# Kernel optimization log

Hardware: AMD Instinct MI355X
Metric: run time of the kernel (lower is better)

## Reference

```python
import jax, jax.numpy as jnp
import numpy as np

NEG_INF = -9e15  # matches torch's -9000000000000000.0 mask value
LEAKY_SLOPE = 0.2  # alpha init arg


def setup_inputs() -> dict:
    key = jax.random.key(0)
    k1, k2, k3, k4, k5, k6 = jax.random.split(key, 6)
    B, N, D = 512, 200, 256
    hidden = jax.random.normal(k1, (B, N, D), dtype=jnp.float32)
    adj = jax.random.randint(k2, (B, N, N), 0, 5, dtype=jnp.int32)
    a0 = jax.random.normal(k3, (D,), dtype=jnp.float32)
    a1 = jax.random.normal(k4, (D,), dtype=jnp.float32)
    a2 = jax.random.normal(k5, (D,), dtype=jnp.float32)
    a3 = jax.random.normal(k6, (D,), dtype=jnp.float32)
    return {"hidden": hidden, "adj": adj, "a0": a0, "a1": a1, "a2": a2, "a3": a3}


def reference(hidden, adj, a0, a1, a2, a3):
    # e_k[b,i,j] = leakyrelu( sum_d h[b,i,d] * h[b,j,d] * a_k[d] )
    # Algebraically identical to the torch (h_i * h_j) @ a_k without
    # materializing the [B, N, N, D] pairwise product tensor.
    def edge_score(a):
        s = jnp.einsum('bid,bjd->bij', hidden * a, hidden)
        return jax.nn.leaky_relu(s, LEAKY_SLOPE)

    e0, e1, e2, e3 = edge_score(a0), edge_score(a1), edge_score(a2), edge_score(a3)
    alpha = jnp.where(adj == 1, e0, NEG_INF)
    alpha = jnp.where(adj == 2, e1, alpha)
    alpha = jnp.where(adj == 3, e2, alpha)
    alpha = jnp.where(adj == 4, e3, alpha)
    alpha = jax.nn.softmax(alpha, axis=-1)  # [B, N, N]
    return jnp.matmul(alpha, hidden)  # [B, N, D]
```

## Files before the change

kernel.cpp:

```cpp
#include <hip/hip_runtime.h>

#define NB 512
#define NN 200
#define ND 256
#define TI 40
#define DC 16
#define NTILE 5
#define NEG_INF -9.0e15f
#define SLOPE 0.2f

#define HJ_STRIDE 204
#define WI_STRIDE 44
#define P1_HJ (DC * HJ_STRIDE)
#define P1_W  (4 * DC * WI_STRIDE)
#define POOLF 8000

__global__ __launch_bounds__(512, 4)
void gat_fused_w3_kernel(const float* __restrict__ h,
                         const int*   __restrict__ adj,
                         const float* __restrict__ a0,
                         const float* __restrict__ a1,
                         const float* __restrict__ a2,
                         const float* __restrict__ a3,
                         float* __restrict__ out)
{
    __shared__ __align__(16) float pool[POOLF];
    float (*sHjT)[HJ_STRIDE]   = (float (*)[HJ_STRIDE])pool;
    float (*sW)[DC][WI_STRIDE] = (float (*)[DC][WI_STRIDE])(pool + P1_HJ);
    float (*sS)[NN]            = (float (*)[NN])pool;

    const int tid = threadIdx.x;
    const int b   = blockIdx.x / NTILE;
    const int it  = blockIdx.x % NTILE;
    const int i0  = it * TI;

    const int ig = tid / 50;
    const int jg = tid % 50;
    const bool active = (ig < 10);

    const float* hb = h + (size_t)b * NN * ND;

    int kk[4][4];
    if (active) {
        #pragma unroll
        for (int ii = 0; ii < 4; ++ii) {
            const int i = i0 + ig * 4 + ii;
            const int4 a4 = *(const int4*)(adj + ((size_t)b * NN + i) * NN + 4 * jg);
            kk[ii][0] = a4.x - 1;
            kk[ii][1] = a4.y - 1;
            kk[ii][2] = a4.z - 1;
            kk[ii][3] = a4.w - 1;
        }
    }

    float acc[4][4][4];
    #pragma unroll
    for (int ii = 0; ii < 4; ++ii)
        #pragma unroll
        for (int jj = 0; jj < 4; ++jj)
            #pragma unroll
            for (int k = 0; k < 4; ++k)
                acc[ii][jj][k] = 0.0f;

    for (int dt = 0; dt < ND; dt += DC) {
        {
            const int row = tid >> 2;
            const int c4  = (tid & 3) * 4;
            for (int j = row; j < NN; j += 128) {
                const float4 v = *(const float4*)(hb + j * ND + dt + c4);
                sHjT[c4 + 0][j] = v.x;
                sHjT[c4 + 1][j] = v.y;
                sHjT[c4 + 2][j] = v.z;
                sHjT[c4 + 3][j] = v.w;
            }
            if (row < TI) {
                const float4 hv  = *(const float4*)(hb + (i0 + row) * ND + dt + c4);
                const float4 va0 = *(const float4*)(a0 + dt + c4);
                const float4 va1 = *(const float4*)(a1 + dt + c4);
                const float4 va2 = *(const float4*)(a2 + dt + c4);
                const float4 va3 = *(const float4*)(a3 + dt + c4);
                sW[0][c4 + 0][row] = hv.x * va0.x;
                sW[0][c4 + 1][row] = hv.y * va0.y;
                sW[0][c4 + 2][row] = hv.z * va0.z;
                sW[0][c4 + 3][row] = hv.w * va0.w;
                sW[1][c4 + 0][row] = hv.x * va1.x;
                sW[1][c4 + 1][row] = hv.y * va1.y;
                sW[1][c4 + 2][row] = hv.z * va1.z;
                sW[1][c4 + 3][row] = hv.w * va1.w;
                sW[2][c4 + 0][row] = hv.x * va2.x;
                sW[2][c4 + 1][row] = hv.y * va2.y;
                sW[2][c4 + 2][row] = hv.z * va2.z;
                sW[2][c4 + 3][row] = hv.w * va2.w;
                sW[3][c4 + 0][row] = hv.x * va3.x;
                sW[3][c4 + 1][row] = hv.y * va3.y;
                sW[3][c4 + 2][row] = hv.z * va3.z;
                sW[3][c4 + 3][row] = hv.w * va3.w;
            }
        }
        __syncthreads();

        if (active) {
            #pragma unroll 4
            for (int dd = 0; dd < DC; ++dd) {
                const float4 hj4 = *(const float4*)&sHjT[dd][4 * jg];
                const float hjv[4] = {hj4.x, hj4.y, hj4.z, hj4.w};
                #pragma unroll
                for (int k = 0; k < 4; ++k) {
                    const float4 w4 = *(const float4*)&sW[k][dd][4 * ig];
                    const float wv_[4] = {w4.x, w4.y, w4.z, w4.w};
                    #pragma unroll
                    for (int ii = 0; ii < 4; ++ii)
                        #pragma unroll
                        for (int jj = 0; jj < 4; ++jj)
                            acc[ii][jj][k] += wv_[ii] * hjv[jj];
                }
            }
        }
        __syncthreads();
    }

    if (active) {
        #pragma unroll
        for (int ii = 0; ii < 4; ++ii) {
            float tmp[4];
            #pragma unroll
            for (int jj = 0; jj < 4; ++jj) {
                const int k = kk[ii][jj];
                float s = (k < 2) ? ((k == 0) ? acc[ii][jj][0] : acc[ii][jj][1])
                                  : ((k == 2) ? acc[ii][jj][2] : acc[ii][jj][3]);
                s = (s >= 0.0f) ? s : SLOPE * s;
                tmp[jj] = (k >= 0) ? s : NEG_INF;
            }
            float4 sv;
            sv.x = tmp[0]; sv.y = tmp[1]; sv.z = tmp[2]; sv.w = tmp[3];
            *(float4*)&sS[ig * 4 + ii][4 * jg] = sv;
        }
    }
    __syncthreads();

    const int wv   = tid >> 6;
    const int lane = tid & 63;
    #pragma unroll
    for (int r = 0; r < 5; ++r) {
        const int row = wv * 5 + r;
        const float v0 = sS[row][lane];
        const float v1 = sS[row][lane + 64];
        const float v2 = sS[row][lane + 128];
        const float v3 = (lane < 8) ? sS[row][lane + 192] : NEG_INF;
        float m = fmaxf(fmaxf(v0, v1), fmaxf(v2, v3));
        #pragma unroll
        for (int off = 32; off > 0; off >>= 1)
            m = fmaxf(m, __shfl_xor(m, off, 64));
        const float p0 = __expf(v0 - m);
        const float p1 = __expf(v1 - m);
        const float p2 = __expf(v2 - m);
        const float p3 = (lane < 8) ? __expf(v3 - m) : 0.0f;
        float l = p0 + p1 + p2 + p3;
        #pragma unroll
        for (int off = 32; off > 0; off >>= 1)
            l += __shfl_xor(l, off, 64);
        const float inv = 1.0f / l;
        sS[row][lane]       = p0 * inv;
        sS[row][lane + 64]  = p1 * inv;
        sS[row][lane + 128] = p2 * inv;
        if (lane < 8) sS[row][lane + 192] = p3 * inv;
    }
    __syncthreads();

    float o[5][4];
    #pragma unroll
    for (int r = 0; r < 5; ++r)
        #pragma unroll
        for (int c = 0; c < 4; ++c)
            o[r][c] = 0.0f;

    const int dcol = lane * 4;
    #pragma unroll 2
    for (int j4 = 0; j4 < NN / 4; ++j4) {
        float alr[5][4];
        #pragma unroll
        for (int r = 0; r < 5; ++r) {
            const float4 a4 = *(const float4*)&sS[wv * 5 + r][4 * j4];
            alr[r][0] = a4.x; alr[r][1] = a4.y; alr[r][2] = a4.z; alr[r][3] = a4.w;
        }
        #pragma unroll
        for (int q = 0; q < 4; ++q) {
            const float4 hv = *(const float4*)(hb + (size_t)(4 * j4 + q) * ND + dcol);
            #pragma unroll
            for (int r = 0; r < 5; ++r) {
                o[r][0] += alr[r][q] * hv.x;
                o[r][1] += alr[r][q] * hv.y;
                o[r][2] += alr[r][q] * hv.z;
                o[r][3] += alr[r][q] * hv.w;
            }
        }
    }

    #pragma unroll
    for (int r = 0; r < 5; ++r) {
        const int i = i0 + wv * 5 + r;
        float4 v;
        v.x = o[r][0]; v.y = o[r][1]; v.z = o[r][2]; v.w = o[r][3];
        *(float4*)(out + ((size_t)b * NN + i) * ND + dcol) = v;
    }
}

extern "C" void kernel_launch(void* const* d_in, const int* in_sizes, int n_in,
                              void* d_out, int out_size, void* d_ws, size_t ws_size,
                              hipStream_t stream) {
    const float* h   = (const float*)d_in[0];
    const int*   adj = (const int*)d_in[1];
    const float* a0  = (const float*)d_in[2];
    const float* a1  = (const float*)d_in[3];
    const float* a2  = (const float*)d_in[4];
    const float* a3  = (const float*)d_in[5];
    float* out = (float*)d_out;

    dim3 grid(NB * NTILE);
    dim3 block(512);
    gat_fused_w3_kernel<<<grid, block, 0, stream>>>(h, adj, a0, a1, a2, a3, out);
}
```

Before: 654.5 us.

## Compute only the adjacency-selected edge score per pair via per-element weight pointers

Instead of accumulating all four edge-type scores per (i,j) pair and selecting one at the end, each thread precomputes, per output element, a pointer into the weight plane chosen by adj. It then accumulates only that single score, cutting FMAs and accumulator registers by four. The weighted i rows are stored row-major so each element reads a float4 over four d values. The cost is one LDS float4 load per output element per four d values, where before one load served sixteen outputs, so LDS bandwidth and bank conflicts from scattered plane addresses may become the limit.

```diff
diff --git a/kernel.cpp b/kernel.cpp
--- a/kernel.cpp
+++ b/kernel.cpp
@@ -10,24 +10,24 @@
 #define SLOPE 0.2f
 
 #define HJ_STRIDE 204
-#define WI_STRIDE 44
+#define WROW 20
+#define WPLANE 808
 #define P1_HJ (DC * HJ_STRIDE)
-#define P1_W  (4 * DC * WI_STRIDE)
 #define POOLF 8000
 
 __global__ __launch_bounds__(512, 4)
-void gat_fused_w3_kernel(const float* __restrict__ h,
-                         const int*   __restrict__ adj,
-                         const float* __restrict__ a0,
-                         const float* __restrict__ a1,
-                         const float* __restrict__ a2,
-                         const float* __restrict__ a3,
-                         float* __restrict__ out)
+void gat_sel_kernel(const float* __restrict__ h,
+                    const int*   __restrict__ adj,
+                    const float* __restrict__ a0,
+                    const float* __restrict__ a1,
+                    const float* __restrict__ a2,
+                    const float* __restrict__ a3,
+                    float* __restrict__ out)
 {
     __shared__ __align__(16) float pool[POOLF];
-    float (*sHjT)[HJ_STRIDE]   = (float (*)[HJ_STRIDE])pool;
-    float (*sW)[DC][WI_STRIDE] = (float (*)[DC][WI_STRIDE])(pool + P1_HJ);
-    float (*sS)[NN]            = (float (*)[NN])pool;
+    float (*sHjT)[HJ_STRIDE] = (float (*)[HJ_STRIDE])pool;
+    float* sW2               = pool + P1_HJ;
+    float (*sS)[NN]          = (float (*)[NN])pool;
 
     const int tid = threadIdx.x;
     const int b   = blockIdx.x / NTILE;
@@ -41,6 +41,11 @@
     const float* hb = h + (size_t)b * NN * ND;
 
     int kk[4][4];
+    #pragma unroll
+    for (int ii = 0; ii < 4; ++ii)
+        #pragma unroll
+        for (int jj = 0; jj < 4; ++jj)
+            kk[ii][jj] = -1;
     if (active) {
         #pragma unroll
         for (int ii = 0; ii < 4; ++ii) {
@@ -53,14 +58,22 @@
         }
     }
 
-    float acc[4][4][4];
+    const float* wp[4][4];
+    #pragma unroll
+    for (int ii = 0; ii < 4; ++ii) {
+        #pragma unroll
+        for (int jj = 0; jj < 4; ++jj) {
+            const int kcl = (kk[ii][jj] >= 0) ? kk[ii][jj] : 0;
+            wp[ii][jj] = sW2 + kcl * WPLANE + (ig * 4 + ii) * WROW;
+        }
+    }
+
+    float acc[4][4];
     #pragma unroll
     for (int ii = 0; ii < 4; ++ii)
         #pragma unroll
         for (int jj = 0; jj < 4; ++jj)
-            #pragma unroll
-            for (int k = 0; k < 4; ++k)
-                acc[ii][jj][k] = 0.0f;
+            acc[ii][jj] = 0.0f;
 
     for (int dt = 0; dt < ND; dt += DC) {
         {
@@ -79,40 +92,40 @@
                 const float4 va1 = *(const float4*)(a1 + dt + c4);
                 const float4 va2 = *(const float4*)(a2 + dt + c4);
                 const float4 va3 = *(const float4*)(a3 + dt + c4);
-                sW[0][c4 + 0][row] = hv.x * va0.x;
-                sW[0][c4 + 1][row] = hv.y * va0.y;
-                sW[0][c4 + 2][row] = hv.z * va0.z;
-                sW[0][c4 + 3][row] = hv.w * va0.w;
-                sW[1][c4 + 0][row] = hv.x * va1.x;
-                sW[1][c4 + 1][row] = hv.y * va1.y;
-                sW[1][c4 + 2][row] = hv.z * va1.z;
-                sW[1][c4 + 3][row] = hv.w * va1.w;
-                sW[2][c4 + 0][row] = hv.x * va2.x;
-                sW[2][c4 + 1][row] = hv.y * va2.y;
-                sW[2][c4 + 2][row] = hv.z * va2.z;
-                sW[2][c4 + 3][row] = hv.w * va2.w;
-                sW[3][c4 + 0][row] = hv.x * va3.x;
-                sW[3][c4 + 1][row] = hv.y * va3.y;
-                sW[3][c4 + 2][row] = hv.z * va3.z;
-                sW[3][c4 + 3][row] = hv.w * va3.w;
+                float4 w;
+                w.x = hv.x * va0.x; w.y = hv.y * va0.y; w.z = hv.z * va0.z; w.w = hv.w * va0.w;
+                *(float4*)(sW2 + 0 * WPLANE + row * WROW + c4) = w;
+                w.x = hv.x * va1.x; w.y = hv.y * va1.y; w.z = hv.z * va1.z; w.w = hv.w * va1.w;
+                *(float4*)(sW2 + 1 * WPLANE + row * WROW + c4) = w;
+                w.x = hv.x * va2.x; w.y = hv.y * va2.y; w.z = hv.z * va2.z; w.w = hv.w * va2.w;
+                *(float4*)(sW2 + 2 * WPLANE + row * WROW + c4) = w;
+                w.x = hv.x * va3.x; w.y = hv.y * va3.y; w.z = hv.z * va3.z; w.w = hv.w * va3.w;
+                *(float4*)(sW2 + 3 * WPLANE + row * WROW + c4) = w;
             }
         }
         __syncthreads();
 
         if (active) {
-            #pragma unroll 4
-            for (int dd = 0; dd < DC; ++dd) {
-                const float4 hj4 = *(const float4*)&sHjT[dd][4 * jg];
-                const float hjv[4] = {hj4.x, hj4.y, hj4.z, hj4.w};
+            #pragma unroll
+            for (int dd4 = 0; dd4 < DC; dd4 += 4) {
+                float hjv[4][4];
                 #pragma unroll
-                for (int k = 0; k < 4; ++k) {
-                    const float4 w4 = *(const float4*)&sW[k][dd][4 * ig];
-                    const float wv_[4] = {w4.x, w4.y, w4.z, w4.w};
+                for (int e = 0; e < 4; ++e) {
+                    const float4 v = *(const float4*)&sHjT[dd4 + e][4 * jg];
+                    hjv[e][0] = v.x; hjv[e][1] = v.y; hjv[e][2] = v.z; hjv[e][3] = v.w;
+                }
+                #pragma unroll
+                for (int ii = 0; ii < 4; ++ii) {
                     #pragma unroll
-                    for (int ii = 0; ii < 4; ++ii)
-                        #pragma unroll
-                        for (int jj = 0; jj < 4; ++jj)
-                            acc[ii][jj][k] += wv_[ii] * hjv[jj];
+                    for (int jj = 0; jj < 4; ++jj) {
+                        const float4 w4 = *(const float4*)(wp[ii][jj] + dd4);
+                        float a = acc[ii][jj];
+                        a += w4.x * hjv[0][jj];
+                        a += w4.y * hjv[1][jj];
+                        a += w4.z * hjv[2][jj];
+                        a += w4.w * hjv[3][jj];
+                        acc[ii][jj] = a;
+                    }
                 }
             }
         }
@@ -125,11 +138,9 @@
             float tmp[4];
             #pragma unroll
             for (int jj = 0; jj < 4; ++jj) {
-                const int k = kk[ii][jj];
-                float s = (k < 2) ? ((k == 0) ? acc[ii][jj][0] : acc[ii][jj][1])
-                                  : ((k == 2) ? acc[ii][jj][2] : acc[ii][jj][3]);
+                float s = acc[ii][jj];
                 s = (s >= 0.0f) ? s : SLOPE * s;
-                tmp[jj] = (k >= 0) ? s : NEG_INF;
+                tmp[jj] = (kk[ii][jj] >= 0) ? s : NEG_INF;
             }
             float4 sv;
             sv.x = tmp[0]; sv.y = tmp[1]; sv.z = tmp[2]; sv.w = tmp[3];
@@ -218,5 +229,5 @@
 
     dim3 grid(NB * NTILE);
     dim3 block(512);
-    gat_fused_w3_kernel<<<grid, block, 0, stream>>>(h, adj, a0, a1, a2, a3, out);
+    gat_sel_kernel<<<grid, block, 0, stream>>>(h, adj, a0, a1, a2, a3, out);
 }
```

After: 869.9 us. +32.9%, slower.
